# Optimization experiments

Hardware: AMD Instinct MI355X
Metric: run time of the kernel (lower is better)

Reference implementation:

```python
import jax, jax.numpy as jnp
import numpy as np

N_USERS = 50000
DEG = 32
N_EDGES = N_USERS * DEG  # 1,600,000
N_SERVERS = 512


def segment_softmax(x, seg, num_segments):
    # PyG-style scatter softmax over segments defined by seg.
    m = jax.ops.segment_max(x, seg, num_segments=num_segments)
    e = jnp.exp(x - m[seg])
    s = jax.ops.segment_sum(e, seg, num_segments=num_segments) + 1e-16
    return e / s[seg]


def setup_inputs() -> dict:
    key = jax.random.key(0)
    k1, k2, k3, k4, k5, k6, k7 = jax.random.split(key, 7)
    # learned parameters (torch.rand init), shape [E, 1]
    task_allocation = jax.random.uniform(k1, (N_EDGES, 1), dtype=jnp.float32)
    power_allocation = jax.random.uniform(k2, (N_EDGES, 1), dtype=jnp.float32)
    comp_allocation = jax.random.uniform(k3, (N_EDGES, 1), dtype=jnp.float32)
    compute_resource = jax.random.uniform(k4, (N_SERVERS,), dtype=jnp.float32) + 0.5
    path_losses = jax.random.uniform(k5, (N_EDGES,), dtype=jnp.float32) + 0.1
    task_size = jax.random.uniform(k6, (N_USERS,), dtype=jnp.float32) + 0.1
    # user index sorted (each user has DEG edges); server index random
    user_index = jnp.repeat(jnp.arange(N_USERS, dtype=jnp.int64), DEG)
    server_index = jax.random.randint(k7, (N_EDGES,), 0, N_SERVERS, dtype=jnp.int64)
    edge_index = jnp.stack([user_index, server_index], axis=0)
    return {
        "compute_resource": compute_resource,
        "path_losses": path_losses,
        "task_size": task_size,
        "edge_index": edge_index,
        "task_allocation": task_allocation,
        "power_allocation": power_allocation,
        "comp_allocation": comp_allocation,
    }


def reference(compute_resource, path_losses, task_size, edge_index,
              task_allocation, power_allocation, comp_allocation):
    epsilon = 1e-9
    extre = 1e-20
    n_users = task_size.shape[0]
    n_servers = compute_resource.shape[0]
    user_index = edge_index[0]
    server_index = edge_index[1]

    task_sche = segment_softmax(task_allocation[:, 0], user_index, n_users)
    power_sche = segment_softmax(power_allocation[:, 0], user_index, n_users)
    comp_sche = segment_softmax(comp_allocation[:, 0], user_index, n_users)

    tasks = task_size[user_index] * task_sche            # [E]
    comp = compute_resource[server_index] * comp_sche     # [E]
    pw = power_sche * path_losses                         # [E]

    # per-server total received power, broadcast back to edges
    pws = jax.ops.segment_sum(pw, server_index, num_segments=n_servers)[server_index]
    interference = pws - pw
    rate = jnp.log2(1.0 + pw / (interference + epsilon))

    time_loss = tasks / (rate + extre) + tasks / (comp + extre)  # [E]
    per_user = jax.ops.segment_sum(time_loss, user_index, num_segments=n_users)
    return per_user.mean()
```

## Files before the change

kernel.cpp:

```cpp
#include <hip/hip_runtime.h>
#include <math.h>

#define NSRV 512
#define NB1  256

__device__ __forceinline__ float quad_sum(float v) {
    int x = __float_as_int(v);
    int y = __builtin_amdgcn_update_dpp(0, x, 0xB1, 0xF, 0xF, true);
    v += __int_as_float(y);
    x = __float_as_int(v);
    y = __builtin_amdgcn_update_dpp(0, x, 0x4E, 0xF, 0xF, true);
    v += __int_as_float(y);
    return v;
}

__device__ __forceinline__ float fast_rcp(float x) {
    return __builtin_amdgcn_rcpf(x);
}

__global__ __launch_bounds__(256) void mmse_pws(
    const float* __restrict__ power_alloc,
    const float* __restrict__ path_losses,
    const int*   __restrict__ server_index,
    float*       __restrict__ pws,
    int n_items) {
    __shared__ float bins[NSRV];
    const int tid = threadIdx.x;
    for (int i = tid; i < NSRV; i += 256) bins[i] = 0.0f;
    __syncthreads();

    const float4* pa4 = (const float4*)power_alloc;
    const float4* pl4 = (const float4*)path_losses;
    const int4*   si4 = (const int4*)server_index;

    const int stride = NB1 * 256;
    for (int t = blockIdx.x * 256 + tid; t < n_items; t += stride) {
        float4 a = pa4[2 * t], b = pa4[2 * t + 1];
        float e0 = __expf(a.x), e1 = __expf(a.y), e2 = __expf(a.z), e3 = __expf(a.w);
        float e4 = __expf(b.x), e5 = __expf(b.y), e6 = __expf(b.z), e7 = __expf(b.w);
        float s   = ((e0 + e1) + (e2 + e3)) + ((e4 + e5) + (e6 + e7));
        float inv = fast_rcp(quad_sum(s) + 1e-16f);

        float4 l0 = pl4[2 * t], l1 = pl4[2 * t + 1];
        int4   s0 = si4[2 * t], s1 = si4[2 * t + 1];

        atomicAdd(&bins[s0.x], e0 * inv * l0.x);
        atomicAdd(&bins[s0.y], e1 * inv * l0.y);
        atomicAdd(&bins[s0.z], e2 * inv * l0.z);
        atomicAdd(&bins[s0.w], e3 * inv * l0.w);
        atomicAdd(&bins[s1.x], e4 * inv * l1.x);
        atomicAdd(&bins[s1.y], e5 * inv * l1.y);
        atomicAdd(&bins[s1.z], e6 * inv * l1.z);
        atomicAdd(&bins[s1.w], e7 * inv * l1.w);
    }
    __syncthreads();

    for (int i = tid; i < NSRV; i += 256) atomicAdd(&pws[i], bins[i]);
}

__global__ __launch_bounds__(256) void mmse_loss(
    const float* __restrict__ task_alloc,
    const float* __restrict__ power_alloc,
    const float* __restrict__ comp_alloc,
    const float* __restrict__ path_losses,
    const int*   __restrict__ server_index,
    const float* __restrict__ task_size,
    const float* __restrict__ compute_resource,
    const float* __restrict__ pws,
    float*       __restrict__ out,
    int n_items, float inv_users) {
    __shared__ float s_pws[NSRV], s_cr[NSRV];
    __shared__ float s_blocksum;
    const int tid = threadIdx.x;

    for (int i = tid; i < NSRV; i += 256) {
        s_pws[i] = pws[i];
        s_cr[i]  = compute_resource[i];
    }
    if (tid == 0) s_blocksum = 0.0f;
    __syncthreads();

    const int t = blockIdx.x * 256 + tid;
    float tl = 0.0f;
    if (t < n_items) {
        const float4* ta4 = (const float4*)task_alloc;
        const float4* pa4 = (const float4*)power_alloc;
        const float4* ca4 = (const float4*)comp_alloc;
        const float4* pl4 = (const float4*)path_losses;
        const int4*   si4 = (const int4*)server_index;

        float4 tA = ta4[2 * t], tB = ta4[2 * t + 1];
        float4 pA = pa4[2 * t], pB = pa4[2 * t + 1];
        float4 cA = ca4[2 * t], cB = ca4[2 * t + 1];
        float4 lA = pl4[2 * t], lB = pl4[2 * t + 1];
        int4   sA = si4[2 * t], sB = si4[2 * t + 1];

        float et[8] = {__expf(tA.x), __expf(tA.y), __expf(tA.z), __expf(tA.w),
                       __expf(tB.x), __expf(tB.y), __expf(tB.z), __expf(tB.w)};
        float ep[8] = {__expf(pA.x), __expf(pA.y), __expf(pA.z), __expf(pA.w),
                       __expf(pB.x), __expf(pB.y), __expf(pB.z), __expf(pB.w)};
        float ec[8] = {__expf(cA.x), __expf(cA.y), __expf(cA.z), __expf(cA.w),
                       __expf(cB.x), __expf(cB.y), __expf(cB.z), __expf(cB.w)};
        float pl[8] = {lA.x, lA.y, lA.z, lA.w, lB.x, lB.y, lB.z, lB.w};
        int   sv[8] = {sA.x, sA.y, sA.z, sA.w, sB.x, sB.y, sB.z, sB.w};

        float st = 0.f, sp = 0.f, sc = 0.f;
#pragma unroll
        for (int k = 0; k < 8; ++k) { st += et[k]; sp += ep[k]; sc += ec[k]; }
        float ist = fast_rcp(quad_sum(st) + 1e-16f);
        float isp = fast_rcp(quad_sum(sp) + 1e-16f);
        float isc = fast_rcp(quad_sum(sc) + 1e-16f);

        const float tsz = task_size[t >> 2];

#pragma unroll
        for (int k = 0; k < 8; ++k) {
            int   srv    = sv[k];
            float tasks  = tsz * (et[k] * ist);
            float comp   = s_cr[srv] * (ec[k] * isc);
            float pwv    = (ep[k] * isp) * pl[k];
            float interf = s_pws[srv] - pwv;
            float rate   = __log2f(1.0f + pwv * fast_rcp(interf + 1e-9f));
            tl += tasks * fast_rcp(rate + 1e-20f) + tasks * fast_rcp(comp + 1e-20f);
        }
    }

    tl = quad_sum(tl);
    if ((tid & 3) == 0 && tl != 0.0f) atomicAdd(&s_blocksum, tl);
    __syncthreads();
    if (tid == 0) atomicAdd(out, s_blocksum * inv_users);
}

extern "C" void kernel_launch(void* const* d_in, const int* in_sizes, int n_in,
                              void* d_out, int out_size, void* d_ws, size_t ws_size,
                              hipStream_t stream) {
    const float* compute_resource = (const float*)d_in[0];
    const float* path_losses      = (const float*)d_in[1];
    const float* task_size        = (const float*)d_in[2];
    const int*   edge_index       = (const int*)d_in[3];
    const float* task_alloc       = (const float*)d_in[4];
    const float* power_alloc      = (const float*)d_in[5];
    const float* comp_alloc       = (const float*)d_in[6];

    const int n_edges = in_sizes[1];
    const int n_users = in_sizes[2];
    const int* server_index = edge_index + n_edges;

    const int n_items = n_edges / 8;
    float* pws = (float*)d_ws;

    mmse_pws<<<NB1, 256, 0, stream>>>(
        power_alloc, path_losses, server_index, pws, n_items);

    const int NB2 = (n_items + 255) / 256;
    mmse_loss<<<NB2, 256, 0, stream>>>(
        task_alloc, power_alloc, comp_alloc, path_losses, server_index,
        task_size, compute_resource, pws, (float*)d_out,
        n_items, 1.0f / (float)n_users);
}
```

Before: 110.3 us.

## Fuse softmax and comp term into first pass, stash tasks and power for second

The first kernel now computes all three segment softmaxes, accumulates the compute-time term and the per-server power histogram. It also writes per-edge tasks and power values to workspace. The second kernel only reads those intermediates plus server indices to evaluate the rate term. This removes the recomputed exps and the duplicate allocation reads, at the cost of writing and re-reading two edge-sized intermediate arrays.

```diff
diff --git a/kernel.cpp b/kernel.cpp
--- a/kernel.cpp
+++ b/kernel.cpp
@@ -3,6 +3,7 @@
 
 #define NSRV 512
 #define NB1  256
+#define TPB1 512
 
 __device__ __forceinline__ float quad_sum(float v) {
     int x = __float_as_int(v);
@@ -18,47 +19,7 @@
     return __builtin_amdgcn_rcpf(x);
 }
 
-__global__ __launch_bounds__(256) void mmse_pws(
-    const float* __restrict__ power_alloc,
-    const float* __restrict__ path_losses,
-    const int*   __restrict__ server_index,
-    float*       __restrict__ pws,
-    int n_items) {
-    __shared__ float bins[NSRV];
-    const int tid = threadIdx.x;
-    for (int i = tid; i < NSRV; i += 256) bins[i] = 0.0f;
-    __syncthreads();
-
-    const float4* pa4 = (const float4*)power_alloc;
-    const float4* pl4 = (const float4*)path_losses;
-    const int4*   si4 = (const int4*)server_index;
-
-    const int stride = NB1 * 256;
-    for (int t = blockIdx.x * 256 + tid; t < n_items; t += stride) {
-        float4 a = pa4[2 * t], b = pa4[2 * t + 1];
-        float e0 = __expf(a.x), e1 = __expf(a.y), e2 = __expf(a.z), e3 = __expf(a.w);
-        float e4 = __expf(b.x), e5 = __expf(b.y), e6 = __expf(b.z), e7 = __expf(b.w);
-        float s   = ((e0 + e1) + (e2 + e3)) + ((e4 + e5) + (e6 + e7));
-        float inv = fast_rcp(quad_sum(s) + 1e-16f);
-
-        float4 l0 = pl4[2 * t], l1 = pl4[2 * t + 1];
-        int4   s0 = si4[2 * t], s1 = si4[2 * t + 1];
-
-        atomicAdd(&bins[s0.x], e0 * inv * l0.x);
-        atomicAdd(&bins[s0.y], e1 * inv * l0.y);
-        atomicAdd(&bins[s0.z], e2 * inv * l0.z);
-        atomicAdd(&bins[s0.w], e3 * inv * l0.w);
-        atomicAdd(&bins[s1.x], e4 * inv * l1.x);
-        atomicAdd(&bins[s1.y], e5 * inv * l1.y);
-        atomicAdd(&bins[s1.z], e6 * inv * l1.z);
-        atomicAdd(&bins[s1.w], e7 * inv * l1.w);
-    }
-    __syncthreads();
-
-    for (int i = tid; i < NSRV; i += 256) atomicAdd(&pws[i], bins[i]);
-}
-
-__global__ __launch_bounds__(256) void mmse_loss(
+__global__ __launch_bounds__(TPB1) void mmse_pass1(
     const float* __restrict__ task_alloc,
     const float* __restrict__ power_alloc,
     const float* __restrict__ comp_alloc,
@@ -66,29 +27,32 @@
     const int*   __restrict__ server_index,
     const float* __restrict__ task_size,
     const float* __restrict__ compute_resource,
-    const float* __restrict__ pws,
+    float*       __restrict__ pws,
+    float*       __restrict__ tasks_st,
+    float*       __restrict__ pw_st,
     float*       __restrict__ out,
     int n_items, float inv_users) {
-    __shared__ float s_pws[NSRV], s_cr[NSRV];
+    __shared__ float bins[NSRV], s_cr[NSRV];
     __shared__ float s_blocksum;
     const int tid = threadIdx.x;
-
-    for (int i = tid; i < NSRV; i += 256) {
-        s_pws[i] = pws[i];
-        s_cr[i]  = compute_resource[i];
+    for (int i = tid; i < NSRV; i += TPB1) {
+        bins[i] = 0.0f;
+        s_cr[i] = compute_resource[i];
     }
     if (tid == 0) s_blocksum = 0.0f;
     __syncthreads();
 
-    const int t = blockIdx.x * 256 + tid;
-    float tl = 0.0f;
-    if (t < n_items) {
-        const float4* ta4 = (const float4*)task_alloc;
-        const float4* pa4 = (const float4*)power_alloc;
-        const float4* ca4 = (const float4*)comp_alloc;
-        const float4* pl4 = (const float4*)path_losses;
-        const int4*   si4 = (const int4*)server_index;
+    const float4* ta4 = (const float4*)task_alloc;
+    const float4* pa4 = (const float4*)power_alloc;
+    const float4* ca4 = (const float4*)comp_alloc;
+    const float4* pl4 = (const float4*)path_losses;
+    const int4*   si4 = (const int4*)server_index;
+    float4* tst4 = (float4*)tasks_st;
+    float4* pst4 = (float4*)pw_st;
 
+    const int gstride = NB1 * TPB1;
+    float comp_term = 0.0f;
+    for (int t = blockIdx.x * TPB1 + tid; t < n_items; t += gstride) {
         float4 tA = ta4[2 * t], tB = ta4[2 * t + 1];
         float4 pA = pa4[2 * t], pB = pa4[2 * t + 1];
         float4 cA = ca4[2 * t], cB = ca4[2 * t + 1];
@@ -113,15 +77,63 @@
 
         const float tsz = task_size[t >> 2];
 
+        float tk[8], pw[8];
 #pragma unroll
         for (int k = 0; k < 8; ++k) {
-            int   srv    = sv[k];
-            float tasks  = tsz * (et[k] * ist);
-            float comp   = s_cr[srv] * (ec[k] * isc);
-            float pwv    = (ep[k] * isp) * pl[k];
-            float interf = s_pws[srv] - pwv;
-            float rate   = __log2f(1.0f + pwv * fast_rcp(interf + 1e-9f));
-            tl += tasks * fast_rcp(rate + 1e-20f) + tasks * fast_rcp(comp + 1e-20f);
+            tk[k] = tsz * (et[k] * ist);
+            pw[k] = (ep[k] * isp) * pl[k];
+            float comp = s_cr[sv[k]] * (ec[k] * isc);
+            comp_term += tk[k] * fast_rcp(comp + 1e-20f);
+            atomicAdd(&bins[sv[k]], pw[k]);
+        }
+        tst4[2 * t]     = make_float4(tk[0], tk[1], tk[2], tk[3]);
+        tst4[2 * t + 1] = make_float4(tk[4], tk[5], tk[6], tk[7]);
+        pst4[2 * t]     = make_float4(pw[0], pw[1], pw[2], pw[3]);
+        pst4[2 * t + 1] = make_float4(pw[4], pw[5], pw[6], pw[7]);
+    }
+
+    comp_term = quad_sum(comp_term);
+    if ((tid & 3) == 0 && comp_term != 0.0f) atomicAdd(&s_blocksum, comp_term);
+    __syncthreads();
+    if (tid == 0) atomicAdd(out, s_blocksum * inv_users);
+
+    for (int i = tid; i < NSRV; i += TPB1) atomicAdd(&pws[i], bins[i]);
+}
+
+__global__ __launch_bounds__(256) void mmse_pass2(
+    const float* __restrict__ tasks_st,
+    const float* __restrict__ pw_st,
+    const int*   __restrict__ server_index,
+    const float* __restrict__ pws,
+    float*       __restrict__ out,
+    int n_items, float inv_users) {
+    __shared__ float s_pws[NSRV];
+    __shared__ float s_blocksum;
+    const int tid = threadIdx.x;
+    for (int i = tid; i < NSRV; i += 256) s_pws[i] = pws[i];
+    if (tid == 0) s_blocksum = 0.0f;
+    __syncthreads();
+
+    const int t = blockIdx.x * 256 + tid;
+    float tl = 0.0f;
+    if (t < n_items) {
+        const float4* tst4 = (const float4*)tasks_st;
+        const float4* pst4 = (const float4*)pw_st;
+        const int4*   si4  = (const int4*)server_index;
+
+        float4 kA = tst4[2 * t], kB = tst4[2 * t + 1];
+        float4 wA = pst4[2 * t], wB = pst4[2 * t + 1];
+        int4   sA = si4[2 * t],  sB = si4[2 * t + 1];
+
+        float tk[8] = {kA.x, kA.y, kA.z, kA.w, kB.x, kB.y, kB.z, kB.w};
+        float pw[8] = {wA.x, wA.y, wA.z, wA.w, wB.x, wB.y, wB.z, wB.w};
+        int   sv[8] = {sA.x, sA.y, sA.z, sA.w, sB.x, sB.y, sB.z, sB.w};
+
+#pragma unroll
+        for (int k = 0; k < 8; ++k) {
+            float interf = s_pws[sv[k]] - pw[k];
+            float rate   = __log2f(1.0f + pw[k] * fast_rcp(interf + 1e-9f));
+            tl += tk[k] * fast_rcp(rate + 1e-20f);
         }
     }
 
@@ -147,14 +159,17 @@
     const int* server_index = edge_index + n_edges;
 
     const int n_items = n_edges / 8;
-    float* pws = (float*)d_ws;
+    float* pws      = (float*)d_ws;
+    float* tasks_st = pws + NSRV;
+    float* pw_st    = tasks_st + n_edges;
+    const float inv_users = 1.0f / (float)n_users;
 
-    mmse_pws<<<NB1, 256, 0, stream>>>(
-        power_alloc, path_losses, server_index, pws, n_items);
+    mmse_pass1<<<NB1, TPB1, 0, stream>>>(
+        task_alloc, power_alloc, comp_alloc, path_losses, server_index,
+        task_size, compute_resource, pws, tasks_st, pw_st, (float*)d_out,
+        n_items, inv_users);
 
     const int NB2 = (n_items + 255) / 256;
-    mmse_loss<<<NB2, 256, 0, stream>>>(
-        task_alloc, power_alloc, comp_alloc, path_losses, server_index,
-        task_size, compute_resource, pws, (float*)d_out,
-        n_items, 1.0f / (float)n_users);
+    mmse_pass2<<<NB2, 256, 0, stream>>>(
+        tasks_st, pw_st, server_index, pws, (float*)d_out, n_items, inv_users);
 }
```

Result: slower. 115.6 us (+4.8%).
